# Kernel tuning notes

Hardware: AMD Instinct MI355X
Metric: run time of the kernel (lower is better)

Reference implementation:

```python
import math
import jax, jax.numpy as jnp
import numpy as np

LMAX = 2


def _cg_complex(j1, m1, j2, m2, j3, m3):
    # Standard (Racah) Clebsch-Gordan coefficient <j1 m1 j2 m2 | j3 m3> for integer l.
    if m1 + m2 != m3 or j3 < abs(j1 - j2) or j3 > j1 + j2:
        return 0.0
    f = math.factorial
    pre = math.sqrt((2 * j3 + 1) * f(j3 + j1 - j2) * f(j3 - j1 + j2) * f(j1 + j2 - j3) / f(j1 + j2 + j3 + 1))
    pre *= math.sqrt(f(j3 + m3) * f(j3 - m3) * f(j1 - m1) * f(j1 + m1) * f(j2 - m2) * f(j2 + m2))
    kmin = max(0, j2 - j3 - m1, j1 + m2 - j3)
    kmax = min(j1 + j2 - j3, j1 - m1, j2 + m2)
    s = 0.0
    for k in range(kmin, kmax + 1):
        s += (-1.0) ** k / (f(k) * f(j1 + j2 - j3 - k) * f(j1 - m1 - k) * f(j2 + m2 - k) * f(j3 - j2 + m1 + k) * f(j3 - j1 - m2 + k))
    return pre * s


def _u_matrix(l):
    # Unitary map from complex SH (Condon-Shortley) to real SH, rows = real mu, cols = complex m.
    U = np.zeros((2 * l + 1, 2 * l + 1), dtype=np.complex128)
    U[l, l] = 1.0
    isq2 = 1.0 / math.sqrt(2.0)
    for m in range(1, l + 1):
        U[l + m, l - m] = isq2
        U[l + m, l + m] = ((-1.0) ** m) * isq2
        U[l - m, l - m] = 1j * isq2
        U[l - m, l + m] = -1j * ((-1.0) ** m) * isq2
    return U


def _real_clebsch_gordan(lmax):
    # Dense real-SH CG tensor over combined s=(l,m) indices, shape [S,S,S], S=(lmax+1)^2.
    S = (lmax + 1) ** 2
    cg = np.zeros((S, S, S))
    for l1 in range(lmax + 1):
        for l2 in range(lmax + 1):
            for l3 in range(abs(l1 - l2), min(lmax, l1 + l2) + 1):
                blk = np.zeros((2 * l1 + 1, 2 * l2 + 1, 2 * l3 + 1))
                for i1, m1 in enumerate(range(-l1, l1 + 1)):
                    for i2, m2 in enumerate(range(-l2, l2 + 1)):
                        for i3, m3 in enumerate(range(-l3, l3 + 1)):
                            blk[i1, i2, i3] = _cg_complex(l1, m1, l2, m2, l3, m3)
                U1, U2, U3 = _u_matrix(l1), _u_matrix(l2), _u_matrix(l3)
                r = np.einsum('am,bn,co,mno->abc', U1, U2, U3.conj(), blk.astype(np.complex128))
                r = r.real if (l1 + l2 + l3) % 2 == 0 else r.imag  # parity-dependent real part
                cg[l1 * l1:(l1 + 1) ** 2, l2 * l2:(l2 + 1) ** 2, l3 * l3:(l3 + 1) ** 2] = r
    return cg


def _sparse_cg(lmax):
    cg = _real_clebsch_gordan(lmax)
    i1, i2, i3 = np.nonzero(np.abs(cg) > 1e-10)
    vals = cg[i1, i2, i3].astype(np.float32)
    widx = np.floor(np.sqrt(i3.astype(np.float64))).astype(np.int32)  # l of output combined index
    return vals, i1.astype(np.int32), i2.astype(np.int32), i3.astype(np.int32), widx


def _spherical_harmonics_l2(d):
    # Real SH up to l=2, 'component' normalization (|x|=1 assumed). Order: (l,m) = (0,0),(1,-1),(1,0),(1,1),(2,-2..2).
    x, y, z = d[..., 0], d[..., 1], d[..., 2]
    s3, s5, s15 = math.sqrt(3.0), math.sqrt(5.0), math.sqrt(15.0)
    return jnp.stack([
        jnp.ones_like(x),
        s3 * y, s3 * z, s3 * x,
        s15 * x * y, s15 * y * z, 0.5 * s5 * (3.0 * z * z - 1.0), s15 * x * z, 0.5 * s15 * (x * x - y * y),
    ], axis=-1)


def setup_inputs():
    N_ATOMS, N_EDGES, N_BASIS, N_RADIAL = 1200, 12000, 128, 20
    S = (LMAX + 1) ** 2
    key = jax.random.key(0)
    ks = jax.random.split(key, 8)
    vals, i1, i2, i3, widx = _sparse_cg(LMAX)
    return {
        'x': jax.random.normal(ks[0], (N_ATOMS, S, N_BASIS), jnp.float32),
        'radial_ij': jax.random.uniform(ks[1], (N_EDGES, N_RADIAL), jnp.float32),
        'dir_ij': jax.random.normal(ks[2], (N_EDGES, 3), jnp.float32),
        'cutoff_ij': jax.random.uniform(ks[3], (N_EDGES, 1), jnp.float32),
        'W_filter': jax.random.normal(ks[6], (N_RADIAL, N_BASIS * (LMAX + 1)), jnp.float32) / math.sqrt(N_RADIAL),
        'b_filter': jnp.zeros((N_BASIS * (LMAX + 1),), jnp.float32),
        'cg_vals': jnp.asarray(vals),
        'idx_i': jax.random.randint(ks[4], (N_EDGES,), 0, N_ATOMS),
        'idx_j': jax.random.randint(ks[5], (N_EDGES,), 0, N_ATOMS),
        'cg_idx_in1': jnp.asarray(i1),
        'cg_idx_in2': jnp.asarray(i2),
        'cg_idx_out': jnp.asarray(i3),
        'w_idx': jnp.asarray(widx),
    }


def reference(x, radial_ij, dir_ij, cutoff_ij, W_filter, b_filter, cg_vals,
              idx_i, idx_j, cg_idx_in1, cg_idx_in2, cg_idx_out, w_idx):
    n_atoms, S, F = x.shape
    E = dir_ij.shape[0]
    d = dir_ij / jnp.linalg.norm(dir_ij, axis=-1, keepdims=True)
    Y = _spherical_harmonics_l2(d)                        # [E, S]
    Wij = (radial_ij @ W_filter + b_filter) * cutoff_ij   # [E, (lmax+1)*F]
    Wij = Wij.reshape(E, LMAX + 1, F)                     # per-l radial filter
    xj = x[idx_j]                                         # [E, S, F] neighbor features
    # Sparse CG tensor-product contraction over combined (l,m) indices.
    v = (Y[:, cg_idx_in2, None] * cg_vals[None, :, None]
         * Wij[:, w_idx, :] * xj[:, cg_idx_in1, :])       # [E, n_cg, F]
    yij = jnp.zeros((E, S, F), v.dtype).at[:, cg_idx_out, :].add(v)
    return jax.ops.segment_sum(yij, idx_i, num_segments=n_atoms)
```

## Files before the change

kernel.cpp:

```cpp
#include <hip/hip_runtime.h>
#include <math.h>


#define S9     9
#define MROW   12
#define MSZ    (S9 * MROW)
#define NF     128
#define NRAD   20
#define CEDGE  8
#define NCHUNK 3
#define CAP    64
#define NCELL  81
#define MAXCG  512

__device__ inline float2 f2fma(float a, float2 b, float2 c) {
    return make_float2(fmaf(a, b.x, c.x), fmaf(a, b.y, c.y));
}

__global__ __launch_bounds__(256) void prep_kernel(
    const int* __restrict__ idx_i, int E, int nbuck,
    const int* __restrict__ cg_i1, const int* __restrict__ cg_i2,
    const int* __restrict__ cg_i3, const float* __restrict__ cg_vals, int ncg,
    int* __restrict__ cnt,
    int* __restrict__ buck,
    int* __restrict__ cellOff,
    int2* __restrict__ cellDat)
{
    const int t = threadIdx.x;
    if ((int)blockIdx.x < nbuck) {
        int e = blockIdx.x * 256 + t;
        if (e < E) {
            int a = idx_i[e];
            int p = atomicAdd(&cnt[a], 1);
            if (p < CAP) buck[a * CAP + p] = e;
        }
        return;
    }
    __shared__ int hist[NCELL];
    __shared__ int cur[NCELL];
    if (t < NCELL) hist[t] = 0;
    __syncthreads();
    for (int k = t; k < ncg; k += 256)
        atomicAdd(&hist[cg_i3[k] * S9 + cg_i1[k]], 1);
    __syncthreads();
    if (t == 0) {
        int run = 0;
        for (int c = 0; c < NCELL; ++c) {
            cellOff[c] = run; cur[c] = run; run += hist[c];
        }
        cellOff[NCELL] = run;
    }
    __syncthreads();
    for (int k = t; k < ncg; k += 256) {
        int cell = cg_i3[k] * S9 + cg_i1[k];
        int p = atomicAdd(&cur[cell], 1);
        cellDat[p] = make_int2(cg_i2[k], __float_as_int(cg_vals[k]));
    }
}

__global__ __launch_bounds__(256) void so3_chunk_kernel(
    const float* __restrict__ x,
    const float* __restrict__ radial,
    const float* __restrict__ dir,
    const float* __restrict__ cutoff,
    const float* __restrict__ Wf,
    const float* __restrict__ bf,
    const int* __restrict__ idx_j,
    const int* __restrict__ cnt,
    const int* __restrict__ buck,
    const int* __restrict__ cellOff,
    const int2* __restrict__ cellDat,
    int ncg, int A,
    float* __restrict__ slots)
{
    const int t    = threadIdx.x;
    const int lane = t & 63;
    const int wid  = t >> 6;
    const int ch   = blockIdx.x * 4 + wid;

    __shared__ __align__(16) float M[4][CEDGE][MSZ];
    __shared__ float Ysh[4][CEDGE][S9];
    __shared__ float radsh[4][CEDGE][NRAD];
    __shared__ float cutsh[4][CEDGE];
    __shared__ int   egsh[4][CEDGE];
    __shared__ int   jsh[4][CEDGE];
    __shared__ int   offsh[NCELL + 1];
    __shared__ int2  datsh[MAXCG];

    int a = 0, q = 0, deg = 0;
    bool active = (ch < A * NCHUNK);
    if (active) {
        a = ch / NCHUNK;
        q = ch - a * NCHUNK;
        deg = min(cnt[a], CAP);
        if (q > 0 && q * CEDGE >= deg) active = false;
    }

    for (int k = t; k <= NCELL; k += 256) offsh[k] = cellOff[k];
    for (int k = t; k < ncg; k += 256) datsh[k] = cellDat[k];
    __syncthreads();
    if (!active) return;

    float2 acc[S9];
    #pragma unroll
    for (int s = 0; s < S9; ++s) acc[s] = make_float2(0.f, 0.f);

    const float2 b0 = ((const float2*)(bf + 0 * NF))[lane];
    const float2 b1 = ((const float2*)(bf + 1 * NF))[lane];
    const float2 b2 = ((const float2*)(bf + 2 * NF))[lane];

    int base = q * CEDGE;
    do {
        const int n = min(CEDGE, deg - base);

        if (lane < CEDGE) {
            int e = 0, jj = a;
            float cut = 0.f;
            float y0 = 0.f, y1 = 0.f, y2 = 0.f, y3 = 0.f, y4 = 0.f,
                  y5 = 0.f, y6 = 0.f, y7 = 0.f, y8 = 0.f;
            if (lane < n) {
                e = buck[a * CAP + base + lane];
                jj = idx_j[e];
                cut = cutoff[e];
                float dx = dir[3 * e], dy = dir[3 * e + 1], dz = dir[3 * e + 2];
                const float inv = rsqrtf(dx * dx + dy * dy + dz * dz);
                dx *= inv; dy *= inv; dz *= inv;
                const float s3c  = 1.7320508075688772f;
                const float s5c  = 2.2360679774997896f;
                const float s15c = 3.8729833462074170f;
                y0 = 1.0f;
                y1 = s3c * dy; y2 = s3c * dz; y3 = s3c * dx;
                y4 = s15c * dx * dy; y5 = s15c * dy * dz;
                y6 = 0.5f * s5c * (3.0f * dz * dz - 1.0f);
                y7 = s15c * dx * dz;
                y8 = 0.5f * s15c * (dx * dx - dy * dy);
            }
            egsh[wid][lane] = e; jsh[wid][lane] = jj; cutsh[wid][lane] = cut;
            Ysh[wid][lane][0] = y0; Ysh[wid][lane][1] = y1; Ysh[wid][lane][2] = y2;
            Ysh[wid][lane][3] = y3; Ysh[wid][lane][4] = y4; Ysh[wid][lane][5] = y5;
            Ysh[wid][lane][6] = y6; Ysh[wid][lane][7] = y7; Ysh[wid][lane][8] = y8;
        }
        for (int qq = lane; qq < CEDGE * NRAD; qq += 64) {
            const int c = qq / NRAD;
            const int r = qq - c * NRAD;
            float v = 0.f;
            if (c < n) v = radial[(size_t)egsh[wid][c] * NRAD + r];
            radsh[wid][c][r] = v;
        }

        float2 w[CEDGE][3];
        #pragma unroll
        for (int c = 0; c < CEDGE; ++c) { w[c][0] = b0; w[c][1] = b1; w[c][2] = b2; }
        #pragma unroll 4
        for (int r = 0; r < NRAD; ++r) {
            const float2* wrow = (const float2*)(Wf + r * (3 * NF));
            const float2 w0 = wrow[lane];
            const float2 w1 = wrow[lane + 64];
            const float2 w2 = wrow[lane + 128];
            #pragma unroll
            for (int c = 0; c < CEDGE; ++c) {
                const float rv = radsh[wid][c][r];
                w[c][0] = f2fma(rv, w0, w[c][0]);
                w[c][1] = f2fma(rv, w1, w[c][1]);
                w[c][2] = f2fma(rv, w2, w[c][2]);
            }
        }
        #pragma unroll
        for (int c = 0; c < CEDGE; ++c) {
            const float cut = cutsh[wid][c];
            w[c][0].x *= cut; w[c][0].y *= cut;
            w[c][1].x *= cut; w[c][1].y *= cut;
            w[c][2].x *= cut; w[c][2].y *= cut;
        }

        #pragma unroll
        for (int cc = 0; cc < 2; ++cc) {
            const int cell = lane + cc * 64;
            if (cell < NCELL) {
                const int s3i = cell / 9;
                const int s1i = cell - 9 * s3i;
                const int o0 = offsh[cell], o1 = offsh[cell + 1];
                float m[CEDGE];
                #pragma unroll
                for (int c = 0; c < CEDGE; ++c) m[c] = 0.f;
                for (int idx = o0; idx < o1; ++idx) {
                    const int2 d = datsh[idx];
                    const float v = __int_as_float(d.y);
                    #pragma unroll
                    for (int c = 0; c < CEDGE; ++c)
                        m[c] = fmaf(v, Ysh[wid][c][d.x], m[c]);
                }
                #pragma unroll
                for (int c = 0; c < CEDGE; ++c) M[wid][c][s3i * MROW + s1i] = m[c];
            }
        }

        #pragma unroll
        for (int c = 0; c < CEDGE; ++c) {
            const int j = __builtin_amdgcn_readfirstlane(jsh[wid][c]);
            const float2* xp = (const float2*)(x + (size_t)j * (S9 * NF)) + lane;
            float2 xj[S9];
            #pragma unroll
            for (int s = 0; s < S9; ++s) xj[s] = xp[s * 64];

            #pragma unroll
            for (int s3 = 0; s3 < S9; ++s3) {
                const float4* mr = (const float4*)&M[wid][c][s3 * MROW];
                const float4 m0 = mr[0];
                const float4 m1 = mr[1];
                const float  m8 = M[wid][c][s3 * MROW + 8];
                float2 tsum = make_float2(0.f, 0.f);
                tsum = f2fma(m0.x, xj[0], tsum);
                tsum = f2fma(m0.y, xj[1], tsum);
                tsum = f2fma(m0.z, xj[2], tsum);
                tsum = f2fma(m0.w, xj[3], tsum);
                tsum = f2fma(m1.x, xj[4], tsum);
                tsum = f2fma(m1.y, xj[5], tsum);
                tsum = f2fma(m1.z, xj[6], tsum);
                tsum = f2fma(m1.w, xj[7], tsum);
                tsum = f2fma(m8,   xj[8], tsum);
                const float2 wl = (s3 == 0) ? w[c][0] : ((s3 < 4) ? w[c][1] : w[c][2]);
                acc[s3].x = fmaf(wl.x, tsum.x, acc[s3].x);
                acc[s3].y = fmaf(wl.y, tsum.y, acc[s3].y);
            }
        }
        base += CEDGE;
    } while (q == NCHUNK - 1 && base < deg);

    float2* sp = (float2*)(slots + (size_t)(a * NCHUNK + q) * (S9 * NF)) + lane;
    #pragma unroll
    for (int s = 0; s < S9; ++s) sp[s * 64] = acc[s];
}

__global__ __launch_bounds__(256) void reduce_kernel(
    const float* __restrict__ slots, const int* __restrict__ cnt, int A,
    float* __restrict__ out)
{
    const int a = blockIdx.x * 4 + (threadIdx.x >> 6);
    if (a >= A) return;
    const int t = threadIdx.x & 63;
    const int deg = min(cnt[a], CAP);
    const int nch = min((deg + CEDGE - 1) / CEDGE, NCHUNK);

    float2 acc[S9];
    #pragma unroll
    for (int s = 0; s < S9; ++s) acc[s] = make_float2(0.f, 0.f);

    for (int q = 0; q < nch; ++q) {
        const float2* sp = (const float2*)(slots + (size_t)(a * NCHUNK + q) * (S9 * NF)) + t;
        #pragma unroll
        for (int s = 0; s < S9; ++s) {
            float2 v = sp[s * 64];
            acc[s].x += v.x; acc[s].y += v.y;
        }
    }
    float2* op = (float2*)(out + (size_t)a * (S9 * NF)) + t;
    #pragma unroll
    for (int s = 0; s < S9; ++s) op[s * 64] = acc[s];
}

__global__ __launch_bounds__(256) void so3_edge_fused(
    const float* __restrict__ x, const float* __restrict__ radial,
    const float* __restrict__ dir, const float* __restrict__ cutoff,
    const float* __restrict__ Wf, const float* __restrict__ bf,
    const float* __restrict__ cg_vals,
    const int* __restrict__ idx_i, const int* __restrict__ idx_j,
    const int* __restrict__ cg_i1, const int* __restrict__ cg_i2,
    const int* __restrict__ cg_i3, int ncg, int E,
    float* __restrict__ out)
{
    const int wid  = threadIdx.x >> 6;
    const int lane = threadIdx.x & 63;
    const int e = blockIdx.x * 4 + wid;
    if (e >= E) return;

    __shared__ __align__(16) float Msh[4][MSZ];
    __shared__ float Ysh[4][S9];

    if (lane < 27) ((float4*)&Msh[wid][0])[lane] = make_float4(0.f, 0.f, 0.f, 0.f);

    float dx = dir[3 * e], dy = dir[3 * e + 1], dz = dir[3 * e + 2];
    const float inv = rsqrtf(dx * dx + dy * dy + dz * dz);
    dx *= inv; dy *= inv; dz *= inv;
    if (lane == 0) {
        const float s3c = 1.7320508075688772f, s5c = 2.2360679774997896f,
                    s15c = 3.8729833462074170f;
        Ysh[wid][0] = 1.0f;
        Ysh[wid][1] = s3c * dy; Ysh[wid][2] = s3c * dz; Ysh[wid][3] = s3c * dx;
        Ysh[wid][4] = s15c * dx * dy; Ysh[wid][5] = s15c * dy * dz;
        Ysh[wid][6] = 0.5f * s5c * (3.0f * dz * dz - 1.0f);
        Ysh[wid][7] = s15c * dx * dz;
        Ysh[wid][8] = 0.5f * s15c * (dx * dx - dy * dy);
    }
    for (int k = lane; k < ncg; k += 64)
        atomicAdd(&Msh[wid][cg_i3[k] * MROW + cg_i1[k]], cg_vals[k] * Ysh[wid][cg_i2[k]]);

    float rad[NRAD];
    #pragma unroll
    for (int r = 0; r < NRAD; ++r) rad[r] = radial[(size_t)e * NRAD + r];
    const float cut = cutoff[e];

    float2 w0 = ((const float2*)(bf + 0 * NF))[lane];
    float2 w1 = ((const float2*)(bf + 1 * NF))[lane];
    float2 w2 = ((const float2*)(bf + 2 * NF))[lane];
    #pragma unroll 4
    for (int r = 0; r < NRAD; ++r) {
        const float2* wrow = (const float2*)(Wf + r * (3 * NF));
        w0 = f2fma(rad[r], wrow[lane], w0);
        w1 = f2fma(rad[r], wrow[lane + 64], w1);
        w2 = f2fma(rad[r], wrow[lane + 128], w2);
    }
    w0.x *= cut; w0.y *= cut; w1.x *= cut; w1.y *= cut; w2.x *= cut; w2.y *= cut;

    const int j = __builtin_amdgcn_readfirstlane(idx_j[e]);
    const float2* xp = (const float2*)(x + (size_t)j * (S9 * NF)) + lane;
    float2 xj[S9];
    #pragma unroll
    for (int s = 0; s < S9; ++s) xj[s] = xp[s * 64];

    const int a = __builtin_amdgcn_readfirstlane(idx_i[e]);
    float* op = out + (size_t)a * (S9 * NF) + 2 * lane;
    #pragma unroll
    for (int s3 = 0; s3 < S9; ++s3) {
        const float4* mr = (const float4*)&Msh[wid][s3 * MROW];
        const float4 m0 = mr[0];
        const float4 m1 = mr[1];
        const float  m8 = Msh[wid][s3 * MROW + 8];
        float2 tsum = make_float2(0.f, 0.f);
        tsum = f2fma(m0.x, xj[0], tsum);
        tsum = f2fma(m0.y, xj[1], tsum);
        tsum = f2fma(m0.z, xj[2], tsum);
        tsum = f2fma(m0.w, xj[3], tsum);
        tsum = f2fma(m1.x, xj[4], tsum);
        tsum = f2fma(m1.y, xj[5], tsum);
        tsum = f2fma(m1.z, xj[6], tsum);
        tsum = f2fma(m1.w, xj[7], tsum);
        tsum = f2fma(m8,   xj[8], tsum);
        const float2 wl = (s3 == 0) ? w0 : ((s3 < 4) ? w1 : w2);
        atomicAdd(&op[s3 * NF],     wl.x * tsum.x);
        atomicAdd(&op[s3 * NF + 1], wl.y * tsum.y);
    }
}

extern "C" void kernel_launch(void* const* d_in, const int* in_sizes, int n_in,
                              void* d_out, int out_size, void* d_ws, size_t ws_size,
                              hipStream_t stream) {
    const float* x       = (const float*)d_in[0];
    const float* radial  = (const float*)d_in[1];
    const float* dir     = (const float*)d_in[2];
    const float* cutoff  = (const float*)d_in[3];
    const float* Wf      = (const float*)d_in[4];
    const float* bf      = (const float*)d_in[5];
    const float* cg_vals = (const float*)d_in[6];
    const int*   idx_i   = (const int*)d_in[7];
    const int*   idx_j   = (const int*)d_in[8];
    const int*   cg_i1   = (const int*)d_in[9];
    const int*   cg_i2   = (const int*)d_in[10];
    const int*   cg_i3   = (const int*)d_in[11];

    const int E   = in_sizes[7];
    const int ncg = in_sizes[6];
    const int A   = in_sizes[0] / (S9 * NF);

    int* cnt      = (int*)d_ws;
    int* cellOff  = cnt + A;
    int* buck     = cellOff + (NCELL + 1);
    size_t ib     = (size_t)(A + NCELL + 1 + A * CAP) * sizeof(int);
    size_t doff   = (ib + 255) & ~(size_t)255;
    int2* cellDat = (int2*)((char*)d_ws + doff);
    size_t soff   = (doff + (size_t)ncg * sizeof(int2) + 255) & ~(size_t)255;
    float* slots  = (float*)((char*)d_ws + soff);
    size_t need   = soff + (size_t)A * NCHUNK * (S9 * NF) * sizeof(float);

    if (ws_size >= need && ncg <= MAXCG) {
        hipMemsetAsync(cnt, 0, (size_t)A * sizeof(int), stream);

        const int nbuck = (E + 255) / 256;
        prep_kernel<<<nbuck + 1, 256, 0, stream>>>(
            idx_i, E, nbuck, cg_i1, cg_i2, cg_i3, cg_vals, ncg,
            cnt, buck, cellOff, cellDat);

        const int nch_total = A * NCHUNK;
        so3_chunk_kernel<<<(nch_total + 3) / 4, 256, 0, stream>>>(
            x, radial, dir, cutoff, Wf, bf, idx_j,
            cnt, buck, cellOff, cellDat, ncg, A, slots);

        reduce_kernel<<<(A + 3) / 4, 256, 0, stream>>>(slots, cnt, A, (float*)d_out);
    } else {
        hipMemsetAsync(d_out, 0, (size_t)out_size * sizeof(float), stream);
        so3_edge_fused<<<(E + 3) / 4, 256, 0, stream>>>(
            x, radial, dir, cutoff, Wf, bf, cg_vals, idx_i, idx_j,
            cg_i1, cg_i2, cg_i3, ncg, E, (float*)d_out);
    }
}
```

Measured before the change: 132.8 us.

## Assign one block per atom with per-edge waves and in-block reduction

Replaces the chunked scheme, where each wave processed 8 edges of an atom and wrote partial sums to global slots for a separate reduce kernel. Now each block owns one atom, its four waves stride over the atom's edges one at a time, and the partial accumulators are combined through shared memory before a single write. This removes the slots buffer, the reduce kernel launch and the global round trip. In exchange it drops the 8-edge batching that amortised the Wf row loads and the Y/CG matrix build, so each edge reloads Wf and rebuilds M, and atoms with low degree leave waves idle.

```diff
diff --git a/kernel.cpp b/kernel.cpp
--- a/kernel.cpp
+++ b/kernel.cpp
@@ -7,8 +7,7 @@
 #define MSZ    (S9 * MROW)
 #define NF     128
 #define NRAD   20
-#define CEDGE  8
-#define NCHUNK 3
+#define WPB    4
 #define CAP    64
 #define NCELL  81
 #define MAXCG  512
@@ -58,7 +57,7 @@
     }
 }
 
-__global__ __launch_bounds__(256) void so3_chunk_kernel(
+__global__ __launch_bounds__(256, 4) void so3_main(
     const float* __restrict__ x,
     const float* __restrict__ radial,
     const float* __restrict__ dir,
@@ -70,36 +69,25 @@
     const int* __restrict__ buck,
     const int* __restrict__ cellOff,
     const int2* __restrict__ cellDat,
-    int ncg, int A,
-    float* __restrict__ slots)
+    int ncg,
+    float* __restrict__ out)
 {
+    const int a    = blockIdx.x;
     const int t    = threadIdx.x;
     const int lane = t & 63;
     const int wid  = t >> 6;
-    const int ch   = blockIdx.x * 4 + wid;
-
-    __shared__ __align__(16) float M[4][CEDGE][MSZ];
-    __shared__ float Ysh[4][CEDGE][S9];
-    __shared__ float radsh[4][CEDGE][NRAD];
-    __shared__ float cutsh[4][CEDGE];
-    __shared__ int   egsh[4][CEDGE];
-    __shared__ int   jsh[4][CEDGE];
+
     __shared__ int   offsh[NCELL + 1];
     __shared__ int2  datsh[MAXCG];
-
-    int a = 0, q = 0, deg = 0;
-    bool active = (ch < A * NCHUNK);
-    if (active) {
-        a = ch / NCHUNK;
-        q = ch - a * NCHUNK;
-        deg = min(cnt[a], CAP);
-        if (q > 0 && q * CEDGE >= deg) active = false;
-    }
+    __shared__ __align__(16) float Msh[WPB][MSZ];
+    __shared__ float Ysh[WPB][S9];
+    __shared__ float red[WPB - 1][S9 * NF];
+
+    const int deg = min(cnt[a], CAP);
 
     for (int k = t; k <= NCELL; k += 256) offsh[k] = cellOff[k];
     for (int k = t; k < ncg; k += 256) datsh[k] = cellDat[k];
     __syncthreads();
-    if (!active) return;
 
     float2 acc[S9];
     #pragma unroll
@@ -109,69 +97,46 @@
     const float2 b1 = ((const float2*)(bf + 1 * NF))[lane];
     const float2 b2 = ((const float2*)(bf + 2 * NF))[lane];
 
-    int base = q * CEDGE;
-    do {
-        const int n = min(CEDGE, deg - base);
-
-        if (lane < CEDGE) {
-            int e = 0, jj = a;
-            float cut = 0.f;
-            float y0 = 0.f, y1 = 0.f, y2 = 0.f, y3 = 0.f, y4 = 0.f,
-                  y5 = 0.f, y6 = 0.f, y7 = 0.f, y8 = 0.f;
-            if (lane < n) {
-                e = buck[a * CAP + base + lane];
-                jj = idx_j[e];
-                cut = cutoff[e];
-                float dx = dir[3 * e], dy = dir[3 * e + 1], dz = dir[3 * e + 2];
-                const float inv = rsqrtf(dx * dx + dy * dy + dz * dz);
-                dx *= inv; dy *= inv; dz *= inv;
+    for (int p = wid; p < deg; p += WPB) {
+        const int e = buck[a * CAP + p];
+        const int j = __builtin_amdgcn_readfirstlane(idx_j[e]);
+        const float cut = cutoff[e];
+
+        {
+            float dx = dir[3 * e], dy = dir[3 * e + 1], dz = dir[3 * e + 2];
+            const float inv = rsqrtf(dx * dx + dy * dy + dz * dz);
+            dx *= inv; dy *= inv; dz *= inv;
+            if (lane == 0) {
                 const float s3c  = 1.7320508075688772f;
                 const float s5c  = 2.2360679774997896f;
                 const float s15c = 3.8729833462074170f;
-                y0 = 1.0f;
-                y1 = s3c * dy; y2 = s3c * dz; y3 = s3c * dx;
-                y4 = s15c * dx * dy; y5 = s15c * dy * dz;
-                y6 = 0.5f * s5c * (3.0f * dz * dz - 1.0f);
-                y7 = s15c * dx * dz;
-                y8 = 0.5f * s15c * (dx * dx - dy * dy);
+                Ysh[wid][0] = 1.0f;
+                Ysh[wid][1] = s3c * dy;
+                Ysh[wid][2] = s3c * dz;
+                Ysh[wid][3] = s3c * dx;
+                Ysh[wid][4] = s15c * dx * dy;
+                Ysh[wid][5] = s15c * dy * dz;
+                Ysh[wid][6] = 0.5f * s5c * (3.0f * dz * dz - 1.0f);
+                Ysh[wid][7] = s15c * dx * dz;
+                Ysh[wid][8] = 0.5f * s15c * (dx * dx - dy * dy);
             }
-            egsh[wid][lane] = e; jsh[wid][lane] = jj; cutsh[wid][lane] = cut;
-            Ysh[wid][lane][0] = y0; Ysh[wid][lane][1] = y1; Ysh[wid][lane][2] = y2;
-            Ysh[wid][lane][3] = y3; Ysh[wid][lane][4] = y4; Ysh[wid][lane][5] = y5;
-            Ysh[wid][lane][6] = y6; Ysh[wid][lane][7] = y7; Ysh[wid][lane][8] = y8;
-        }
-        for (int qq = lane; qq < CEDGE * NRAD; qq += 64) {
-            const int c = qq / NRAD;
-            const int r = qq - c * NRAD;
-            float v = 0.f;
-            if (c < n) v = radial[(size_t)egsh[wid][c] * NRAD + r];
-            radsh[wid][c][r] = v;
-        }
-
-        float2 w[CEDGE][3];
-        #pragma unroll
-        for (int c = 0; c < CEDGE; ++c) { w[c][0] = b0; w[c][1] = b1; w[c][2] = b2; }
+        }
+
+        float rad[NRAD];
+        #pragma unroll
+        for (int r = 0; r < NRAD; ++r) rad[r] = radial[(size_t)e * NRAD + r];
+
+        float2 w0 = b0, w1 = b1, w2 = b2;
         #pragma unroll 4
         for (int r = 0; r < NRAD; ++r) {
             const float2* wrow = (const float2*)(Wf + r * (3 * NF));
-            const float2 w0 = wrow[lane];
-            const float2 w1 = wrow[lane + 64];
-            const float2 w2 = wrow[lane + 128];
-            #pragma unroll
-            for (int c = 0; c < CEDGE; ++c) {
-                const float rv = radsh[wid][c][r];
-                w[c][0] = f2fma(rv, w0, w[c][0]);
-                w[c][1] = f2fma(rv, w1, w[c][1]);
-                w[c][2] = f2fma(rv, w2, w[c][2]);
-            }
-        }
-        #pragma unroll
-        for (int c = 0; c < CEDGE; ++c) {
-            const float cut = cutsh[wid][c];
-            w[c][0].x *= cut; w[c][0].y *= cut;
-            w[c][1].x *= cut; w[c][1].y *= cut;
-            w[c][2].x *= cut; w[c][2].y *= cut;
-        }
+            w0 = f2fma(rad[r], wrow[lane],       w0);
+            w1 = f2fma(rad[r], wrow[lane + 64],  w1);
+            w2 = f2fma(rad[r], wrow[lane + 128], w2);
+        }
+        w0.x *= cut; w0.y *= cut;
+        w1.x *= cut; w1.y *= cut;
+        w2.x *= cut; w2.y *= cut;
 
         #pragma unroll
         for (int cc = 0; cc < 2; ++cc) {
@@ -180,83 +145,62 @@
                 const int s3i = cell / 9;
                 const int s1i = cell - 9 * s3i;
                 const int o0 = offsh[cell], o1 = offsh[cell + 1];
-                float m[CEDGE];
-                #pragma unroll
-                for (int c = 0; c < CEDGE; ++c) m[c] = 0.f;
+                float m = 0.f;
                 for (int idx = o0; idx < o1; ++idx) {
                     const int2 d = datsh[idx];
-                    const float v = __int_as_float(d.y);
-                    #pragma unroll
-                    for (int c = 0; c < CEDGE; ++c)
-                        m[c] = fmaf(v, Ysh[wid][c][d.x], m[c]);
+                    m = fmaf(__int_as_float(d.y), Ysh[wid][d.x], m);
                 }
-                #pragma unroll
-                for (int c = 0; c < CEDGE; ++c) M[wid][c][s3i * MROW + s1i] = m[c];
+                Msh[wid][s3i * MROW + s1i] = m;
             }
         }
 
-        #pragma unroll
-        for (int c = 0; c < CEDGE; ++c) {
-            const int j = __builtin_amdgcn_readfirstlane(jsh[wid][c]);
-            const float2* xp = (const float2*)(x + (size_t)j * (S9 * NF)) + lane;
-            float2 xj[S9];
+        const float2* xp = (const float2*)(x + (size_t)j * (S9 * NF)) + lane;
+        float2 xj[S9];
+        #pragma unroll
+        for (int s = 0; s < S9; ++s) xj[s] = xp[s * 64];
+
+        #pragma unroll
+        for (int s3 = 0; s3 < S9; ++s3) {
+            const float4* mr = (const float4*)&Msh[wid][s3 * MROW];
+            const float4 m0 = mr[0];
+            const float4 m1 = mr[1];
+            const float  m8 = Msh[wid][s3 * MROW + 8];
+            float2 tsum = make_float2(0.f, 0.f);
+            tsum = f2fma(m0.x, xj[0], tsum);
+            tsum = f2fma(m0.y, xj[1], tsum);
+            tsum = f2fma(m0.z, xj[2], tsum);
+            tsum = f2fma(m0.w, xj[3], tsum);
+            tsum = f2fma(m1.x, xj[4], tsum);
+            tsum = f2fma(m1.y, xj[5], tsum);
+            tsum = f2fma(m1.z, xj[6], tsum);
+            tsum = f2fma(m1.w, xj[7], tsum);
+            tsum = f2fma(m8,   xj[8], tsum);
+            const float2 wl = (s3 == 0) ? w0 : ((s3 < 4) ? w1 : w2);
+            acc[s3].x = fmaf(wl.x, tsum.x, acc[s3].x);
+            acc[s3].y = fmaf(wl.y, tsum.y, acc[s3].y);
+        }
+    }
+
+    if (wid > 0) {
+        float2* rp = (float2*)&red[wid - 1][0];
+        #pragma unroll
+        for (int s = 0; s < S9; ++s) rp[s * 64 + lane] = acc[s];
+    }
+    __syncthreads();
+    if (wid == 0) {
+        #pragma unroll
+        for (int r2 = 0; r2 < WPB - 1; ++r2) {
+            const float2* rp = (const float2*)&red[r2][0];
             #pragma unroll
-            for (int s = 0; s < S9; ++s) xj[s] = xp[s * 64];
-
-            #pragma unroll
-            for (int s3 = 0; s3 < S9; ++s3) {
-                const float4* mr = (const float4*)&M[wid][c][s3 * MROW];
-                const float4 m0 = mr[0];
-                const float4 m1 = mr[1];
-                const float  m8 = M[wid][c][s3 * MROW + 8];
-                float2 tsum = make_float2(0.f, 0.f);
-                tsum = f2fma(m0.x, xj[0], tsum);
-                tsum = f2fma(m0.y, xj[1], tsum);
-                tsum = f2fma(m0.z, xj[2], tsum);
-                tsum = f2fma(m0.w, xj[3], tsum);
-                tsum = f2fma(m1.x, xj[4], tsum);
-                tsum = f2fma(m1.y, xj[5], tsum);
-                tsum = f2fma(m1.z, xj[6], tsum);
-                tsum = f2fma(m1.w, xj[7], tsum);
-                tsum = f2fma(m8,   xj[8], tsum);
-                const float2 wl = (s3 == 0) ? w[c][0] : ((s3 < 4) ? w[c][1] : w[c][2]);
-                acc[s3].x = fmaf(wl.x, tsum.x, acc[s3].x);
-                acc[s3].y = fmaf(wl.y, tsum.y, acc[s3].y);
+            for (int s = 0; s < S9; ++s) {
+                float2 v = rp[s * 64 + lane];
+                acc[s].x += v.x; acc[s].y += v.y;
             }
         }
-        base += CEDGE;
-    } while (q == NCHUNK - 1 && base < deg);
-
-    float2* sp = (float2*)(slots + (size_t)(a * NCHUNK + q) * (S9 * NF)) + lane;
-    #pragma unroll
-    for (int s = 0; s < S9; ++s) sp[s * 64] = acc[s];
-}
-
-__global__ __launch_bounds__(256) void reduce_kernel(
-    const float* __restrict__ slots, const int* __restrict__ cnt, int A,
-    float* __restrict__ out)
-{
-    const int a = blockIdx.x * 4 + (threadIdx.x >> 6);
-    if (a >= A) return;
-    const int t = threadIdx.x & 63;
-    const int deg = min(cnt[a], CAP);
-    const int nch = min((deg + CEDGE - 1) / CEDGE, NCHUNK);
-
-    float2 acc[S9];
-    #pragma unroll
-    for (int s = 0; s < S9; ++s) acc[s] = make_float2(0.f, 0.f);
-
-    for (int q = 0; q < nch; ++q) {
-        const float2* sp = (const float2*)(slots + (size_t)(a * NCHUNK + q) * (S9 * NF)) + t;
-        #pragma unroll
-        for (int s = 0; s < S9; ++s) {
-            float2 v = sp[s * 64];
-            acc[s].x += v.x; acc[s].y += v.y;
-        }
-    }
-    float2* op = (float2*)(out + (size_t)a * (S9 * NF)) + t;
-    #pragma unroll
-    for (int s = 0; s < S9; ++s) op[s * 64] = acc[s];
+        float2* op = (float2*)(out + (size_t)a * (S9 * NF)) + lane;
+        #pragma unroll
+        for (int s = 0; s < S9; ++s) op[s * 64] = acc[s];
+    }
 }
 
 __global__ __launch_bounds__(256) void so3_edge_fused(
@@ -368,9 +312,7 @@
     size_t ib     = (size_t)(A + NCELL + 1 + A * CAP) * sizeof(int);
     size_t doff   = (ib + 255) & ~(size_t)255;
     int2* cellDat = (int2*)((char*)d_ws + doff);
-    size_t soff   = (doff + (size_t)ncg * sizeof(int2) + 255) & ~(size_t)255;
-    float* slots  = (float*)((char*)d_ws + soff);
-    size_t need   = soff + (size_t)A * NCHUNK * (S9 * NF) * sizeof(float);
+    size_t need   = doff + (size_t)ncg * sizeof(int2);
 
     if (ws_size >= need && ncg <= MAXCG) {
         hipMemsetAsync(cnt, 0, (size_t)A * sizeof(int), stream);
@@ -380,12 +322,9 @@
             idx_i, E, nbuck, cg_i1, cg_i2, cg_i3, cg_vals, ncg,
             cnt, buck, cellOff, cellDat);
 
-        const int nch_total = A * NCHUNK;
-        so3_chunk_kernel<<<(nch_total + 3) / 4, 256, 0, stream>>>(
+        so3_main<<<A, 256, 0, stream>>>(
             x, radial, dir, cutoff, Wf, bf, idx_j,
-            cnt, buck, cellOff, cellDat, ncg, A, slots);
-
-        reduce_kernel<<<(A + 3) / 4, 256, 0, stream>>>(slots, cnt, A, (float*)d_out);
+            cnt, buck, cellOff, cellDat, ncg, (float*)d_out);
     } else {
         hipMemsetAsync(d_out, 0, (size_t)out_size * sizeof(float), stream);
         so3_edge_fused<<<(E + 3) / 4, 256, 0, stream>>>(
```

Measured after the change: 148.7 us. +12.0%, slower.
